# Optimization experiments

Hardware: AMD Instinct MI355X
Metric: run time of the kernel (lower is better)

## Reference

```python
import jax, jax.numpy as jnp
import numpy as np

V = 1_000_000   # input_size (item vocab)
H = 128         # hidden_size
BASKET_LEN = 200


def setup_inputs() -> dict:
    key = jax.random.key(0)
    k1, k2, k3, k4, k5 = jax.random.split(key, 5)
    s = 1.0 / np.sqrt(H)  # PyTorch GRU init scale
    return {
        "basket": jax.random.randint(k1, (BASKET_LEN,), 0, V),
        "hidden": jnp.zeros((1, 1, H), dtype=jnp.float32),
        "emb_table": jax.random.normal(k2, (V, H), dtype=jnp.float32),
        "w_ih": jax.random.uniform(k3, (3 * H, H), dtype=jnp.float32, minval=-s, maxval=s),
        "w_hh": jax.random.uniform(k4, (3 * H, H), dtype=jnp.float32, minval=-s, maxval=s),
        "b_ih": jax.random.uniform(k5, (3 * H,), dtype=jnp.float32, minval=-s, maxval=s),
        "b_hh": jax.random.uniform(jax.random.fold_in(k5, 1), (3 * H,), dtype=jnp.float32, minval=-s, maxval=s),
    }


def reference(basket, hidden, emb_table, w_ih, w_hh, b_ih, b_hh):
    # embedding-bag sum over basket items, then the quirky /hidden_size average
    emb = jnp.sum(emb_table[basket], axis=0) / H              # [H]
    h = hidden[0, 0]                                          # [H]
    # single-step single-layer PyTorch GRU cell
    gi = w_ih @ emb + b_ih                                    # [3H]
    gh = w_hh @ h + b_hh                                      # [3H]
    i_r, i_z, i_n = jnp.split(gi, 3)
    h_r, h_z, h_n = jnp.split(gh, 3)
    r = jax.nn.sigmoid(i_r + h_r)
    z = jax.nn.sigmoid(i_z + h_z)
    n = jnp.tanh(i_n + r * h_n)
    h_new = (1.0 - z) * n + z * h                             # [H]
    out = h_new.reshape(1, 1, H)                              # output [seq=1, batch=1, H]
    return out, out.reshape(1, 1, H)  # (output, hidden) — identical for 1-layer 1-step GRU
```

## Files before the change

kernel.cpp:

```cpp
#include <hip/hip_runtime.h>
#include <math.h>

#define H 128
#define BASKET 200
#define CHUNKS 8
#define PER (BASKET / CHUNKS)

__global__ __launch_bounds__(1024)
void gru_encoder_fused(const int* __restrict__ basket,
                       const float* __restrict__ hidden,
                       const float* __restrict__ emb_table,
                       const float* __restrict__ w_ih,
                       const float* __restrict__ w_hh,
                       const float* __restrict__ b_ih,
                       const float* __restrict__ b_hh,
                       float* __restrict__ out)
{
    __shared__ int   s_idx[BASKET];
    __shared__ float s_part[CHUNKS][H];
    __shared__ float s_emb[H];
    __shared__ float s_h[H];
    __shared__ float s_gi[3 * H];
    __shared__ float s_gh[3 * H];

    const int t = threadIdx.x;

    if (t < BASKET) s_idx[t] = basket[t];
    __syncthreads();

    {
        const int h = t & (H - 1);
        const int c = t >> 7;
        float acc = 0.0f;
        #pragma unroll
        for (int i = 0; i < PER; ++i) {
            const int idx = s_idx[c * PER + i];
            acc += emb_table[(size_t)idx * H + h];
        }
        s_part[c][h] = acc;
    }
    __syncthreads();

    if (t < H) {
        float s = 0.0f;
        #pragma unroll
        for (int c = 0; c < CHUNKS; ++c) s += s_part[c][t];
        s_emb[t] = s * (1.0f / (float)H);
        s_h[t]   = hidden[t];
    }
    __syncthreads();

    if (t < 2 * 3 * H) {
        const bool ih  = (t < 3 * H);
        const int  row = ih ? t : t - 3 * H;
        const float* __restrict__ w   = ih ? w_ih  : w_hh;
        const float* __restrict__ vec = ih ? s_emb : s_h;
        const float4* __restrict__ w4 = (const float4*)(w + (size_t)row * H);
        float acc = ih ? b_ih[row] : b_hh[row];
        #pragma unroll
        for (int k = 0; k < H / 4; ++k) {
            const float4 wv = w4[k];
            acc += wv.x * vec[4 * k + 0]
                 + wv.y * vec[4 * k + 1]
                 + wv.z * vec[4 * k + 2]
                 + wv.w * vec[4 * k + 3];
        }
        if (ih) s_gi[row] = acc; else s_gh[row] = acc;
    }
    __syncthreads();

    if (t < H) {
        const float ir = s_gi[t], iz = s_gi[H + t], inn = s_gi[2 * H + t];
        const float hr = s_gh[t], hz = s_gh[H + t], hnn = s_gh[2 * H + t];
        const float r  = 1.0f / (1.0f + expf(-(ir + hr)));
        const float z  = 1.0f / (1.0f + expf(-(iz + hz)));
        const float n  = tanhf(inn + r * hnn);
        const float hv = s_h[t];
        const float hnew = (1.0f - z) * n + z * hv;
        out[t]     = hnew;
        out[H + t] = hnew;
    }
}

extern "C" void kernel_launch(void* const* d_in, const int* in_sizes, int n_in,
                              void* d_out, int out_size, void* d_ws, size_t ws_size,
                              hipStream_t stream) {
    const int*   basket    = (const int*)  d_in[0];
    const float* hidden    = (const float*)d_in[1];
    const float* emb_table = (const float*)d_in[2];
    const float* w_ih      = (const float*)d_in[3];
    const float* w_hh      = (const float*)d_in[4];
    const float* b_ih      = (const float*)d_in[5];
    const float* b_hh      = (const float*)d_in[6];
    float* out = (float*)d_out;

    gru_encoder_fused<<<1, 1024, 0, stream>>>(basket, hidden, emb_table,
                                              w_ih, w_hh, b_ih, b_hh, out);
}
```

Baseline: 564.7 us.

## Split GRU encoder into parallel gather kernel with cache-warming blocks and matvec kernel

The embedding gather moves into a first kernel that spreads the basket rows across 8 blocks and writes partial sums to workspace. That kernel's extra 24 blocks read all of w_ih, w_hh, the biases and hidden so they sit in cache before the second kernel runs. The second kernel reduces the partials, runs the matvec with float4 shared-memory loads and applies the gates. This trades the single-block serial gather for an extra kernel launch, a global-memory round trip, and redundant weight reads in the warming blocks.

New measurement: 581.2 us. +2.9%, slower.

```diff
diff --git a/kernel.cpp b/kernel.cpp
--- a/kernel.cpp
+++ b/kernel.cpp
@@ -3,67 +3,96 @@
 
 #define H 128
 #define BASKET 200
-#define CHUNKS 8
-#define PER (BASKET / CHUNKS)
+#define NGATHER 8
+#define ROWS_PER_BLK 25
+#define R3H (3 * H)
 
-__global__ __launch_bounds__(1024)
-void gru_encoder_fused(const int* __restrict__ basket,
-                       const float* __restrict__ hidden,
-                       const float* __restrict__ emb_table,
-                       const float* __restrict__ w_ih,
-                       const float* __restrict__ w_hh,
-                       const float* __restrict__ b_ih,
-                       const float* __restrict__ b_hh,
-                       float* __restrict__ out)
+#define WS_PART 0
+#define WS_DUMP 4096
+
+__global__ __launch_bounds__(256)
+void k1_gather_warm(const int* __restrict__ basket,
+                    const float* __restrict__ emb_table,
+                    const float* __restrict__ w_ih,
+                    const float* __restrict__ w_hh,
+                    const float* __restrict__ b_ih,
+                    const float* __restrict__ b_hh,
+                    const float* __restrict__ hidden,
+                    float* __restrict__ ws)
 {
-    __shared__ int   s_idx[BASKET];
-    __shared__ float s_part[CHUNKS][H];
-    __shared__ float s_emb[H];
-    __shared__ float s_h[H];
-    __shared__ float s_gi[3 * H];
-    __shared__ float s_gh[3 * H];
+    const int b = blockIdx.x;
+    const int t = threadIdx.x;
+
+    if (b < NGATHER) {
+        __shared__ int   s_idx[ROWS_PER_BLK];
+        __shared__ float s_sub[2][H];
+        if (t < ROWS_PER_BLK) s_idx[t] = basket[b * ROWS_PER_BLK + t];
+        __syncthreads();
+        const int h = t & (H - 1);
+        const int c = t >> 7;
+        const int lo = c ? 13 : 0;
+        const int hi = c ? 25 : 13;
+        float acc = 0.0f;
+        for (int i = lo; i < hi; ++i)
+            acc += emb_table[(size_t)s_idx[i] * H + h];
+        s_sub[c][h] = acc;
+        __syncthreads();
+        if (t < H) ws[WS_PART + b * H + t] = s_sub[0][t] + s_sub[1][t];
+    } else {
+        const float4* a4 = (const float4*)w_ih;
+        const float4* b4 = (const float4*)w_hh;
+        const int n4 = R3H * H / 4;
+        float4 acc = {0.f, 0.f, 0.f, 0.f};
+        for (int i = t; i < n4; i += 256) {
+            const float4 x = a4[i];
+            const float4 y = b4[i];
+            acc.x += x.x + y.x; acc.y += x.y + y.y;
+            acc.z += x.z + y.z; acc.w += x.w + y.w;
+        }
+        float s = acc.x + acc.y + acc.z + acc.w;
+        for (int i = t; i < R3H; i += 256) s += b_ih[i] + b_hh[i];
+        if (t < H) s += hidden[t];
+        ws[WS_DUMP + b] = s;
+    }
+}
+
+__global__ __launch_bounds__(768)
+void k2_matvec_gates(const float* __restrict__ hidden,
+                     const float* __restrict__ w_ih,
+                     const float* __restrict__ w_hh,
+                     const float* __restrict__ b_ih,
+                     const float* __restrict__ b_hh,
+                     const float* __restrict__ ws,
+                     float* __restrict__ out)
+{
+    __shared__ __align__(16) float s_emb[H];
+    __shared__ __align__(16) float s_h[H];
+    __shared__ float s_gi[R3H];
+    __shared__ float s_gh[R3H];
 
     const int t = threadIdx.x;
-
-    if (t < BASKET) s_idx[t] = basket[t];
-    __syncthreads();
-
-    {
-        const int h = t & (H - 1);
-        const int c = t >> 7;
-        float acc = 0.0f;
-        #pragma unroll
-        for (int i = 0; i < PER; ++i) {
-            const int idx = s_idx[c * PER + i];
-            acc += emb_table[(size_t)idx * H + h];
-        }
-        s_part[c][h] = acc;
-    }
-    __syncthreads();
 
     if (t < H) {
         float s = 0.0f;
         #pragma unroll
-        for (int c = 0; c < CHUNKS; ++c) s += s_part[c][t];
+        for (int b = 0; b < NGATHER; ++b) s += ws[WS_PART + b * H + t];
         s_emb[t] = s * (1.0f / (float)H);
         s_h[t]   = hidden[t];
     }
     __syncthreads();
 
-    if (t < 2 * 3 * H) {
-        const bool ih  = (t < 3 * H);
-        const int  row = ih ? t : t - 3 * H;
-        const float* __restrict__ w   = ih ? w_ih  : w_hh;
-        const float* __restrict__ vec = ih ? s_emb : s_h;
+    {
+        const bool ih  = (t < R3H);
+        const int  row = ih ? t : t - R3H;
+        const float* __restrict__ w = ih ? w_ih : w_hh;
         const float4* __restrict__ w4 = (const float4*)(w + (size_t)row * H);
+        const float4* __restrict__ v4 = (const float4*)(ih ? s_emb : s_h);
         float acc = ih ? b_ih[row] : b_hh[row];
         #pragma unroll
         for (int k = 0; k < H / 4; ++k) {
             const float4 wv = w4[k];
-            acc += wv.x * vec[4 * k + 0]
-                 + wv.y * vec[4 * k + 1]
-                 + wv.z * vec[4 * k + 2]
-                 + wv.w * vec[4 * k + 3];
+            const float4 vv = v4[k];
+            acc += wv.x * vv.x + wv.y * vv.y + wv.z * vv.z + wv.w * vv.w;
         }
         if (ih) s_gi[row] = acc; else s_gh[row] = acc;
     }
@@ -93,7 +122,10 @@
     const float* b_ih      = (const float*)d_in[5];
     const float* b_hh      = (const float*)d_in[6];
     float* out = (float*)d_out;
+    float* ws  = (float*)d_ws;
 
-    gru_encoder_fused<<<1, 1024, 0, stream>>>(basket, hidden, emb_table,
-                                              w_ih, w_hh, b_ih, b_hh, out);
+    k1_gather_warm<<<32, 256, 0, stream>>>(basket, emb_table, w_ih, w_hh,
+                                           b_ih, b_hh, hidden, ws);
+    k2_matvec_gates<<<1, 768, 0, stream>>>(hidden, w_ih, w_hh, b_ih, b_hh,
+                                           ws, out);
 }
```
